# Performance work log

Measured on AMD Instinct MI355X. Metric: run time of the kernel, lower is better.

## Reference

```python
import jax, jax.numpy as jnp
import numpy as np

NU, NI = 16384, 8192          # num_users, num_items
DK, DM = 64, 64               # embed_k, embed_k_multimod
DV, DT = 4096, 384            # visual / textual feature dims
TOP_K = 10
N_LAYERS = 1                  # item-graph propagation layers
N_UI_LAYERS = 2               # user-item LGConv layers
L_M = 0.7
E = 524288                    # user-item interactions (doubled to symmetric edges)


def build_sim(x):
    # cosine similarity: row-normalize then x @ x.T  -> [N, N]
    xn = x / jnp.linalg.norm(x, axis=-1, keepdims=True)
    return xn @ xn.T


def build_knn(sim, k):
    # keep top-k values per row, zero elsewhere (torch topk + scatter_)
    vals, idx = jax.lax.top_k(sim, k)
    rows = jnp.arange(sim.shape[0])[:, None]
    return jnp.zeros_like(sim).at[rows, idx].set(vals)


def normalized_laplacian(adj):
    # D^{-1/2} A D^{-1/2}; inf (zero-degree) -> 0, applied as row/col scaling
    d = adj.sum(-1)
    dis = jnp.where(d > 0, jax.lax.rsqrt(jnp.where(d > 0, d, 1.0)), 0.0)
    return adj * dis[:, None] * dis[None, :]


def l2_normalize(x, axis=-1, eps=1e-12):
    n = jnp.linalg.norm(x, axis=axis, keepdims=True)
    return x / jnp.maximum(n, eps)


def setup_inputs() -> dict:
    key = jax.random.key(0)
    ks = jax.random.split(key, 8)
    Gu = jax.random.normal(ks[0], (NU, DK), jnp.float32) * 0.1
    Gi = jax.random.normal(ks[1], (NI, DK), jnp.float32) * 0.1
    feat_v = jax.random.normal(ks[2], (NI, DV), jnp.float32)
    feat_t = jax.random.normal(ks[3], (NI, DT), jnp.float32)
    W_v = jax.random.normal(ks[4], (DV, DM), jnp.float32) / np.sqrt(DV)
    b_v = jnp.zeros((DM,), jnp.float32)
    W_t = jax.random.normal(ks[5], (DT, DM), jnp.float32) / np.sqrt(DT)
    b_t = jnp.zeros((DM,), jnp.float32)
    importance_weights = jnp.full((2,), 0.5, jnp.float32)
    # precomputed per-modality normalized laplacians from raw (detached) features
    Sim_v = normalized_laplacian(build_knn(build_sim(feat_v), TOP_K))
    Sim_t = normalized_laplacian(build_knn(build_sim(feat_t), TOP_K))
    # symmetric bipartite user-item edge list (items offset by NU)
    u = jax.random.randint(ks[6], (E,), 0, NU)
    i = jax.random.randint(ks[7], (E,), 0, NI) + NU
    edge_index = jnp.stack([jnp.concatenate([u, i]), jnp.concatenate([i, u])])
    return dict(Gu=Gu, Gi=Gi, feat_v=feat_v, feat_t=feat_t, W_v=W_v, b_v=b_v,
                W_t=W_t, b_t=b_t, importance_weights=importance_weights,
                Sim_v=Sim_v, Sim_t=Sim_t, edge_index=edge_index)


def propagate(Gu, Gi, feat_v, feat_t, W_v, b_v, W_t, b_t,
              importance_weights, Sim_v, Sim_t, edge_index):
    w = jax.nn.softmax(importance_weights)
    learned = jnp.zeros((NI, NI), jnp.float32)
    original = jnp.zeros((NI, NI), jnp.float32)
    for m, (feat, W, b, Sim) in enumerate(
            [(feat_v, W_v, b_v, Sim_v), (feat_t, W_t, b_t, Sim_t)]):
        proj = feat @ W + b                                  # [NI, DM]
        learned = learned + w[m] * build_knn(build_sim(proj), TOP_K)
        original = original + w[m] * Sim
    Si = (1.0 - L_M) * normalized_laplacian(learned) + L_M * original
    # item-graph propagation
    item_emb = Gi
    for _ in range(N_LAYERS):
        item_emb = Si @ item_emb                              # [NI, DK]
    # user-item LGConv (normalize=False => plain sum aggregation)
    src, dst = edge_index[0], edge_index[1]
    all_emb = [jnp.concatenate([Gu, Gi], 0)]                  # [NU+NI, DK]
    for _ in range(N_UI_LAYERS):
        agg = jax.ops.segment_sum(all_emb[-1][src], dst, num_segments=NU + NI)
        all_emb.append(l2_normalize(agg, axis=1))
    mean_emb = jnp.stack(all_emb, 1).mean(1)
    gu, gi = mean_emb[:NU], mean_emb[NU:]
    return gu, gi + l2_normalize(item_emb, axis=1)


def reference(Gu, Gi, feat_v, feat_t, W_v, b_v, W_t, b_t,
              importance_weights, Sim_v, Sim_t, edge_index):
    return propagate(Gu, Gi, feat_v, feat_t, W_v, b_v, W_t, b_t,
                     importance_weights, Sim_v, Sim_t, edge_index)
```

## Files before the change

kernel.cpp:

```cpp
#include <hip/hip_runtime.h>
#include <hip/hip_bf16.h>

#define NU 16384
#define NI 8192
#define TOPK 10
#define NTOT (NU + NI)
#define OCAP 64
#define NSEG 4
#define CSEG (NI / NSEG)
#define NGRP 512
#define MAXSEL 16

typedef short short8v __attribute__((ext_vector_type(8)));
typedef float float4v __attribute__((ext_vector_type(4)));

__device__ __forceinline__ float warp64_sum(float v) {
#pragma unroll
  for (int m = 32; m >= 1; m >>= 1) v += __shfl_xor(v, m);
  return v;
}

__device__ __forceinline__ unsigned int umap(float f) {
  unsigned int b = __float_as_uint(f);
  return b ^ ((b & 0x80000000u) ? 0xFFFFFFFFu : 0x80000000u);
}

__global__ __launch_bounds__(256) void fused_proj_hist_kernel(
    const float* __restrict__ feat, const float* __restrict__ W,
    float* __restrict__ partial, int D, int kchunk,
    const int* __restrict__ dst, int* __restrict__ deg, int nedge) {
  __shared__ float sA[64][64];
  __shared__ float sB[64][68];
  const int tid = threadIdx.x;
  if (blockIdx.x >= 1024) {
    int e = (blockIdx.x - 1024) * 256 + tid;
    if (e < nedge) atomicAdd(&deg[dst[e]], 1);
    return;
  }
  const int pb = blockIdx.x;
  const int r0 = (pb & 127) * 64;
  const int ks = pb >> 7;
  const int rg = tid >> 4, cg = tid & 15;
  const int rA = tid & 63, kgA = (tid >> 6) * 16;
  const int kB = tid & 63, cbB = (tid >> 6) * 16;
  const int kbeg = ks * kchunk, kend = kbeg + kchunk;
  float4 pa[4], pb4[4];
  {
    const float* fp = feat + (size_t)(r0 + rA) * D + kbeg + kgA;
    pa[0] = *(const float4*)(fp + 0);  pa[1] = *(const float4*)(fp + 4);
    pa[2] = *(const float4*)(fp + 8);  pa[3] = *(const float4*)(fp + 12);
    const float* wp = W + (size_t)(kbeg + kB) * 64 + cbB;
    pb4[0] = *(const float4*)(wp + 0);  pb4[1] = *(const float4*)(wp + 4);
    pb4[2] = *(const float4*)(wp + 8);  pb4[3] = *(const float4*)(wp + 12);
  }
  float acc[4][4] = {{0,0,0,0},{0,0,0,0},{0,0,0,0},{0,0,0,0}};
  for (int kc = kbeg; kc < kend; kc += 64) {
#pragma unroll
    for (int i = 0; i < 4; ++i) {
      sA[kgA + 4*i + 0][rA] = pa[i].x;
      sA[kgA + 4*i + 1][rA] = pa[i].y;
      sA[kgA + 4*i + 2][rA] = pa[i].z;
      sA[kgA + 4*i + 3][rA] = pa[i].w;
      *(float4*)&sB[kB][cbB + 4*i] = pb4[i];
    }
    __syncthreads();
    if (kc + 64 < kend) {
      const float* fp = feat + (size_t)(r0 + rA) * D + kc + 64 + kgA;
      pa[0] = *(const float4*)(fp + 0);  pa[1] = *(const float4*)(fp + 4);
      pa[2] = *(const float4*)(fp + 8);  pa[3] = *(const float4*)(fp + 12);
      const float* wp = W + (size_t)(kc + 64 + kB) * 64 + cbB;
      pb4[0] = *(const float4*)(wp + 0);  pb4[1] = *(const float4*)(wp + 4);
      pb4[2] = *(const float4*)(wp + 8);  pb4[3] = *(const float4*)(wp + 12);
    }
#pragma unroll 8
    for (int k = 0; k < 64; ++k) {
      float4 a = *(const float4*)&sA[k][rg * 4];
      float4 b = *(const float4*)&sB[k][cg * 4];
      acc[0][0] += a.x * b.x; acc[0][1] += a.x * b.y; acc[0][2] += a.x * b.z; acc[0][3] += a.x * b.w;
      acc[1][0] += a.y * b.x; acc[1][1] += a.y * b.y; acc[1][2] += a.y * b.z; acc[1][3] += a.y * b.w;
      acc[2][0] += a.z * b.x; acc[2][1] += a.z * b.y; acc[2][2] += a.z * b.z; acc[2][3] += a.z * b.w;
      acc[3][0] += a.w * b.x; acc[3][1] += a.w * b.y; acc[3][2] += a.w * b.z; acc[3][3] += a.w * b.w;
    }
    __syncthreads();
  }
#pragma unroll
  for (int rr = 0; rr < 4; ++rr) {
    float4 o = make_float4(acc[rr][0], acc[rr][1], acc[rr][2], acc[rr][3]);
    *(float4*)(partial + ((size_t)ks * NI + r0 + rg * 4 + rr) * 64 + cg * 4) = o;
  }
}

__global__ __launch_bounds__(256) void fused_projT_reduceV_scanA_kernel(
    const float* __restrict__ feat, const float* __restrict__ W,
    float* __restrict__ partialT,
    const float* __restrict__ partialV, const float* __restrict__ bv,
    float* __restrict__ xn, ushort* __restrict__ hi, ushort* __restrict__ lo,
    const int* __restrict__ deg, int* __restrict__ loc, int* __restrict__ bsum) {
  __shared__ float sA[64][64];
  __shared__ float sB[64][68];
  __shared__ int s[256];
  const int tid = threadIdx.x;
  const int bid = blockIdx.x;
  if (bid >= 768 && bid < 2816) {
    const int row = (bid - 768) * 4 + (tid >> 6);
    const int col = tid & 63;
    float acc = bv[col];
#pragma unroll
    for (int ks = 0; ks < 8; ++ks)
      acc += partialV[((size_t)ks * NI + row) * 64 + col];
    float ss = warp64_sum(acc * acc);
    float v = acc * (1.0f / sqrtf(ss));
    xn[(size_t)row * 64 + col] = v;
    __hip_bfloat16 hb = __float2bfloat16(v);
    float hf = __bfloat162float(hb);
    __hip_bfloat16 lb = __float2bfloat16(v - hf);
    hi[(size_t)row * 64 + col] = *(ushort*)&hb;
    lo[(size_t)row * 64 + col] = *(ushort*)&lb;
    return;
  }
  if (bid >= 2816) {
    int gid = (bid - 2816) * 256 + tid;
    int x = deg[gid];
    s[tid] = x;
    __syncthreads();
    for (int off = 1; off < 256; off <<= 1) {
      int t = (tid >= off) ? s[tid - off] : 0;
      __syncthreads();
      s[tid] += t;
      __syncthreads();
    }
    loc[gid] = s[tid] - x;
    if (tid == 255) bsum[bid - 2816] = s[255];
    return;
  }
  const int pb = bid;
  const int r0 = (pb & 127) * 64;
  const int ks = pb >> 7;
  const int rg = tid >> 4, cg = tid & 15;
  const int rA = tid & 63, kgA = (tid >> 6) * 16;
  const int kB = tid & 63, cbB = (tid >> 6) * 16;
  const int kbeg = ks * 64;
  const int D = 384;
  float4 pa[4], pb4[4];
  {
    const float* fp = feat + (size_t)(r0 + rA) * D + kbeg + kgA;
    pa[0] = *(const float4*)(fp + 0);  pa[1] = *(const float4*)(fp + 4);
    pa[2] = *(const float4*)(fp + 8);  pa[3] = *(const float4*)(fp + 12);
    const float* wp = W + (size_t)(kbeg + kB) * 64 + cbB;
    pb4[0] = *(const float4*)(wp + 0);  pb4[1] = *(const float4*)(wp + 4);
    pb4[2] = *(const float4*)(wp + 8);  pb4[3] = *(const float4*)(wp + 12);
  }
  float acc[4][4] = {{0,0,0,0},{0,0,0,0},{0,0,0,0},{0,0,0,0}};
#pragma unroll
  for (int i = 0; i < 4; ++i) {
    sA[kgA + 4*i + 0][rA] = pa[i].x;
    sA[kgA + 4*i + 1][rA] = pa[i].y;
    sA[kgA + 4*i + 2][rA] = pa[i].z;
    sA[kgA + 4*i + 3][rA] = pa[i].w;
    *(float4*)&sB[kB][cbB + 4*i] = pb4[i];
  }
  __syncthreads();
#pragma unroll 8
  for (int k = 0; k < 64; ++k) {
    float4 a = *(const float4*)&sA[k][rg * 4];
    float4 b = *(const float4*)&sB[k][cg * 4];
    acc[0][0] += a.x * b.x; acc[0][1] += a.x * b.y; acc[0][2] += a.x * b.z; acc[0][3] += a.x * b.w;
    acc[1][0] += a.y * b.x; acc[1][1] += a.y * b.y; acc[1][2] += a.y * b.z; acc[1][3] += a.y * b.w;
    acc[2][0] += a.z * b.x; acc[2][1] += a.z * b.y; acc[2][2] += a.z * b.z; acc[2][3] += a.z * b.w;
    acc[3][0] += a.w * b.x; acc[3][1] += a.w * b.y; acc[3][2] += a.w * b.z; acc[3][3] += a.w * b.w;
  }
#pragma unroll
  for (int rr = 0; rr < 4; ++rr) {
    float4 o = make_float4(acc[rr][0], acc[rr][1], acc[rr][2], acc[rr][3]);
    *(float4*)(partialT + ((size_t)ks * NI + r0 + rg * 4 + rr) * 64 + cg * 4) = o;
  }
}

__global__ __launch_bounds__(256) void fused_reduceT_scanC_kernel(
    const float* __restrict__ partialT, const float* __restrict__ bt,
    float* __restrict__ xn, ushort* __restrict__ hi, ushort* __restrict__ lo,
    const int* __restrict__ loc, const int* __restrict__ bsum,
    int* __restrict__ row_ptr, int* __restrict__ cursor, int n) {
  const int tid = threadIdx.x;
  const int bid = blockIdx.x;
  if (bid >= 2048) {
    int gid = (bid - 2048) * 256 + tid;
    if (gid > n) return;
    int blk = gid >> 8;
    int off = 0;
    for (int b2 = 0; b2 < blk; ++b2) off += bsum[b2];
    if (gid == n) { row_ptr[n] = off; return; }
    int v = off + loc[gid];
    row_ptr[gid] = v;
    cursor[gid] = v;
    return;
  }
  const int row = bid * 4 + (tid >> 6);
  const int col = tid & 63;
  float acc = bt[col];
#pragma unroll
  for (int ks = 0; ks < 6; ++ks)
    acc += partialT[((size_t)ks * NI + row) * 64 + col];
  float ss = warp64_sum(acc * acc);
  float v = acc * (1.0f / sqrtf(ss));
  xn[(size_t)row * 64 + col] = v;
  __hip_bfloat16 hb = __float2bfloat16(v);
  float hf = __bfloat162float(hb);
  __hip_bfloat16 lb = __float2bfloat16(v - hf);
  hi[(size_t)row * 64 + col] = *(ushort*)&hb;
  lo[(size_t)row * 64 + col] = *(ushort*)&lb;
}

__global__ __launch_bounds__(256) void fused_sim_kernel(
    const float* __restrict__ Sv, const float* __restrict__ St,
    const float* __restrict__ iw, int* __restrict__ ocols,
    float* __restrict__ ow, int* __restrict__ ocnt,
    const ushort* __restrict__ hiV, const ushort* __restrict__ loV,
    const ushort* __restrict__ hiT, const ushort* __restrict__ loT,
    float* __restrict__ tmax,
    const int* __restrict__ esrc, const int* __restrict__ edst,
    int* __restrict__ cursor, int* __restrict__ csr, int nedge) {
  __shared__ ushort sH[64][64];
  __shared__ ushort sL[64][64];
  const int tid = threadIdx.x;
  const int bid = blockIdx.x;
  if (bid >= 1024 && bid < 3072) {
    const int lane = tid & 63;
    const int row = (bid - 1024) * 4 + (tid >> 6);
    float ea = expf(iw[0]), eb = expf(iw[1]);
    float wA = 0.7f * ea / (ea + eb), wB = 0.7f * eb / (ea + eb);
    int cnt = 0;
    int* oc = ocols + (size_t)row * OCAP;
    float* op = ow + (size_t)row * OCAP;
#pragma unroll 1
    for (int m = 0; m < 2; ++m) {
      const float* S = m ? St : Sv;
      float wgt = m ? wB : wA;
      const float4* rp = (const float4*)(S + (size_t)row * NI);
      float4 buf0 = rp[0 * 64 + lane];
      float4 buf1 = rp[1 * 64 + lane];
      float4 buf2 = rp[2 * 64 + lane];
      float4 buf3 = rp[3 * 64 + lane];
#pragma unroll 1
      for (int it0 = 0; it0 < NI / 256; it0 += 4) {
        float4 n0, n1, n2, n3;
        if (it0 + 4 < NI / 256) {
          n0 = rp[(it0 + 4) * 64 + lane];
          n1 = rp[(it0 + 5) * 64 + lane];
          n2 = rp[(it0 + 6) * 64 + lane];
          n3 = rp[(it0 + 7) * 64 + lane];
        }
#pragma unroll
        for (int k = 0; k < 4; ++k) {
          float4 cur = (k == 0) ? buf0 : (k == 1) ? buf1 : (k == 2) ? buf2 : buf3;
          const int it = it0 + k;
          bool anynz = (cur.x != 0.0f) | (cur.y != 0.0f) | (cur.z != 0.0f) | (cur.w != 0.0f);
          if (__ballot(anynz) != 0ull) {
            int cb = it * 256 + lane * 4;
#pragma unroll
            for (int j = 0; j < 4; ++j) {
              float x = (j == 0) ? cur.x : (j == 1) ? cur.y : (j == 2) ? cur.z : cur.w;
              bool nz = (x != 0.0f);
              unsigned long long mk = __ballot(nz);
              int pre = __popcll(mk & ((1ull << lane) - 1ull));
              if (nz) {
                int p = cnt + pre;
                if (p < OCAP) { oc[p] = cb + j; op[p] = wgt * x; }
              }
              cnt += __popcll(mk);
            }
          }
        }
        buf0 = n0; buf1 = n1; buf2 = n2; buf3 = n3;
      }
    }
    if (lane == 0) ocnt[row] = (cnt < OCAP) ? cnt : OCAP;
    return;
  }
  if (bid >= 3072) {
    int e = (bid - 3072) * 256 + tid;
    if (e < nedge) {
      int p = atomicAdd(&cursor[edst[e]], 1);
      csr[p] = esrc[e];
    }
    return;
  }
  const int t2 = bid;
  const int m = t2 >> 9;
  const int rest = t2 & 511;
  const int seg = rest >> 7;
  const int r_base = (rest & 127) * 64;
  const ushort* hi = m ? hiT : hiV;
  const ushort* lo = m ? loT : loV;
  const int c_base = seg * CSEG;
  const int wave = tid >> 6, lane = tid & 63;
  const int lr = lane & 15, lg = lane >> 4;
  const int my_row = r_base + wave * 16 + lr;
  short8v bh[2], bl[2];
  {
    const ushort* rp = hi + (size_t)my_row * 64 + lg * 8;
    bh[0] = *(const short8v*)(rp);
    bh[1] = *(const short8v*)(rp + 32);
    const ushort* rp2 = lo + (size_t)my_row * 64 + lg * 8;
    bl[0] = *(const short8v*)(rp2);
    bl[1] = *(const short8v*)(rp2 + 32);
  }
  float* tbase = tmax + ((size_t)m * NI + my_row) * NGRP + seg * (CSEG / 16);
  const int sc = tid >> 2, sq = (tid & 3) * 32;
  const int sw = (sc & 7) << 4;
  for (int c0 = 0; c0 < CSEG; c0 += 64) {
    __syncthreads();
    const char* gh = (const char*)(hi + (size_t)(c_base + c0 + sc) * 64);
    const char* gl2 = (const char*)(lo + (size_t)(c_base + c0 + sc) * 64);
    *(float4*)((char*)&sH[sc][0] + (sq ^ sw)) = *(const float4*)(gh + sq);
    *(float4*)((char*)&sH[sc][0] + ((sq + 16) ^ sw)) = *(const float4*)(gh + sq + 16);
    *(float4*)((char*)&sL[sc][0] + (sq ^ sw)) = *(const float4*)(gl2 + sq);
    *(float4*)((char*)&sL[sc][0] + ((sq + 16) ^ sw)) = *(const float4*)(gl2 + sq + 16);
    __syncthreads();
#pragma unroll
    for (int s = 0; s < 4; ++s) {
      const int ca = s * 16 + lr;
      const int cw = (ca & 7) << 4;
      const int kb0 = (lg * 16) ^ cw;
      const int kb1 = (lg * 16 + 64) ^ cw;
      short8v ah0 = *(const short8v*)((const char*)&sH[ca][0] + kb0);
      short8v ah1 = *(const short8v*)((const char*)&sH[ca][0] + kb1);
      short8v al0 = *(const short8v*)((const char*)&sL[ca][0] + kb0);
      short8v al1 = *(const short8v*)((const char*)&sL[ca][0] + kb1);
      float4v acc = {0.f, 0.f, 0.f, 0.f};
      acc = __builtin_amdgcn_mfma_f32_16x16x32_bf16(ah0, bh[0], acc, 0, 0, 0);
      acc = __builtin_amdgcn_mfma_f32_16x16x32_bf16(ah1, bh[1], acc, 0, 0, 0);
      acc = __builtin_amdgcn_mfma_f32_16x16x32_bf16(ah0, bl[0], acc, 0, 0, 0);
      acc = __builtin_amdgcn_mfma_f32_16x16x32_bf16(ah1, bl[1], acc, 0, 0, 0);
      acc = __builtin_amdgcn_mfma_f32_16x16x32_bf16(al0, bh[0], acc, 0, 0, 0);
      acc = __builtin_amdgcn_mfma_f32_16x16x32_bf16(al1, bh[1], acc, 0, 0, 0);
      float gm = fmaxf(fmaxf(acc[0], acc[1]), fmaxf(acc[2], acc[3]));
      gm = fmaxf(gm, __shfl_xor(gm, 16));
      gm = fmaxf(gm, __shfl_xor(gm, 32));
      if (lg == 0) tbase[(c0 >> 4) + s] = gm;
    }
  }
}

__global__ __launch_bounds__(256) void tile_rescore_kernel(
    const float* __restrict__ xn_v, const float* __restrict__ xn_t,
    const float* __restrict__ tmax,
    float* __restrict__ tkvV, int* __restrict__ tkiV,
    float* __restrict__ tkvT, int* __restrict__ tkiT) {
  const int bid = blockIdx.x;
  const int m = bid >> 13;
  const int row = bid & (NI - 1);
  const float* xn = m ? xn_t : xn_v;
  const int tid = threadIdx.x;
  __shared__ int ssel[MAXSEL];
  __shared__ float sval[MAXSEL * 16];
  __shared__ int scol[MAXSEL * 16];
  __shared__ float lv[32];
  __shared__ int lc[32];
  __shared__ int lnum;
  const int grp = tid >> 4, l16 = tid & 15;
  float4 rq = ((const float4*)(xn + (size_t)row * 64))[l16];
  if (tid < 64) {
    const int lane = tid;
    const float4* tmr4 = (const float4*)(tmax + ((size_t)m * NI + row) * NGRP);
    float4 t0 = tmr4[lane];
    float4 t1 = tmr4[64 + lane];
    unsigned int uv[8] = {umap(t0.x), umap(t0.y), umap(t0.z), umap(t0.w),
                          umap(t1.x), umap(t1.y), umap(t1.z), umap(t1.w)};
    unsigned long long blo = 0, bhi = 0x100000000ull;
    unsigned int taub = 0;
    for (int it = 0; it < 34; ++it) {
      unsigned int mid = (unsigned int)((blo + bhi) >> 1);
      int cnt = 0;
#pragma unroll
      for (int j = 0; j < 8; ++j) cnt += __popcll(__ballot(uv[j] >= mid));
      if (cnt >= 12) {
        taub = mid;
        if (cnt <= MAXSEL) break;
        blo = (unsigned long long)mid + 1;
      } else {
        bhi = mid;
      }
      if (blo >= bhi) break;
    }
    unsigned long long bj[8];
    int base[8];
    int tot = 0;
#pragma unroll
    for (int j = 0; j < 8; ++j) {
      bj[j] = __ballot(uv[j] >= taub);
      base[j] = tot;
      tot += __popcll(bj[j]);
    }
    if (lane < MAXSEL) ssel[lane] = -1;
    unsigned long long ltm = (1ull << lane) - 1ull;
#pragma unroll
    for (int j = 0; j < 8; ++j) {
      if (uv[j] >= taub) {
        int pos = base[j] + __popcll(bj[j] & ltm);
        if (pos < MAXSEL) {
          int g = (j < 4) ? (lane * 4 + j) : (256 + lane * 4 + (j - 4));
          ssel[pos] = g;
        }
      }
    }
  }
  __syncthreads();
  for (int it = 0; it < MAXSEL; ++it) {
    int gsel = ssel[it];
    bool valid = (gsel >= 0);
    int c = valid ? (gsel * 16 + grp) : 0;
    float4 x4 = ((const float4*)(xn + (size_t)c * 64))[l16];
    float s = rq.x * x4.x + rq.y * x4.y + rq.z * x4.z + rq.w * x4.w;
    s += __shfl_xor(s, 1);
    s += __shfl_xor(s, 2);
    s += __shfl_xor(s, 4);
    s += __shfl_xor(s, 8);
    if (l16 == 0) {
      sval[it * 16 + grp] = valid ? s : -3.0e38f;
      scol[it * 16 + grp] = valid ? c : 0x7fffffff;
    }
  }
  __syncthreads();
  if (tid < 64) {
    const int lane = tid;
    float fv[4];
    int fc[4];
    unsigned int uv4[4];
#pragma unroll
    for (int k = 0; k < 4; ++k) {
      fv[k] = sval[lane + 64 * k];
      fc[k] = scol[lane + 64 * k];
      uv4[k] = umap(fv[k]);
    }
    unsigned long long blo = 0, bhi = 0x100000000ull;
    unsigned int taub = 0;
    for (int it = 0; it < 34; ++it) {
      unsigned int mid = (unsigned int)((blo + bhi) >> 1);
      int cnt = 0;
#pragma unroll
      for (int k = 0; k < 4; ++k) cnt += __popcll(__ballot(uv4[k] >= mid));
      if (cnt >= TOPK) {
        taub = mid;
        if (cnt == TOPK) break;
        blo = (unsigned long long)mid + 1;
      } else {
        bhi = mid;
      }
      if (blo >= bhi) break;
    }
    unsigned long long bk[4];
    int base[4];
    int tot = 0;
#pragma unroll
    for (int k = 0; k < 4; ++k) {
      bk[k] = __ballot(uv4[k] >= taub);
      base[k] = tot;
      tot += __popcll(bk[k]);
    }
    float* tv = m ? tkvT : tkvV;
    int* ti = m ? tkiT : tkiV;
    unsigned long long ltm = (1ull << lane) - 1ull;
    if (tot == TOPK) {
#pragma unroll
      for (int k = 0; k < 4; ++k) {
        if (uv4[k] >= taub) {
          int pos = base[k] + __popcll(bk[k] & ltm);
          tv[(size_t)row * TOPK + pos] = fv[k];
          ti[(size_t)row * TOPK + pos] = fc[k];
        }
      }
    } else {
#pragma unroll
      for (int k = 0; k < 4; ++k) {
        if (uv4[k] >= taub) {
          int pos = base[k] + __popcll(bk[k] & ltm);
          if (pos < 32) { lv[pos] = fv[k]; lc[pos] = fc[k]; }
        }
      }
      if (lane == 0) lnum = (tot < 32) ? tot : 32;
      if (lane == 0) {
        int n = lnum;
        unsigned int used = 0;
        for (int q = 0; q < TOPK; ++q) {
          float bv = -3.0e38f;
          int bc = 0x7fffffff, bi = -1;
          for (int i2 = 0; i2 < n; ++i2) {
            if (used & (1u << i2)) continue;
            if (lv[i2] > bv || (lv[i2] == bv && lc[i2] < bc)) {
              bv = lv[i2]; bc = lc[i2]; bi = i2;
            }
          }
          used |= (1u << bi);
          tv[(size_t)row * TOPK + q] = bv;
          ti[(size_t)row * TOPK + q] = bc;
        }
      }
    }
  }
}

__global__ void dis_kernel(const float* __restrict__ tkv_v, const float* __restrict__ tkv_t,
                           const float* __restrict__ iw, float* __restrict__ dis) {
  int r = blockIdx.x * blockDim.x + threadIdx.x;
  if (r >= NI) return;
  float ea = expf(iw[0]), eb = expf(iw[1]);
  float w0 = ea / (ea + eb), w1 = eb / (ea + eb);
  float s0 = 0.f, s1 = 0.f;
  for (int j = 0; j < TOPK; ++j) { s0 += tkv_v[r * TOPK + j]; s1 += tkv_t[r * TOPK + j]; }
  float d = w0 * s0 + w1 * s1;
  dis[r] = (d > 0.0f) ? (1.0f / sqrtf(d)) : 0.0f;
}

__global__ __launch_bounds__(256) void fused_item_segsum_kernel(
    const float* __restrict__ Gi,
    const float* __restrict__ tkv_v, const int* __restrict__ tki_v,
    const float* __restrict__ tkv_t, const int* __restrict__ tki_t,
    const float* __restrict__ dis, const int* __restrict__ ocols,
    const float* __restrict__ ow, const int* __restrict__ ocnt,
    const float* __restrict__ iw, float* __restrict__ nitem,
    const float* __restrict__ Gu, const int* __restrict__ row_ptr,
    const int* __restrict__ csr, float* __restrict__ e1b) {
  const int tid = threadIdx.x;
  const int d = tid & 63;
  if (blockIdx.x >= 2048) {
    const int row = (blockIdx.x - 2048) * 4 + (tid >> 6);
    int a = row_ptr[row], bnd = row_ptr[row + 1];
    float acc = 0.0f;
    for (int e = a; e < bnd; ++e) {
      int s = csr[e];
      const float* sp = (s < NU) ? (Gu + (size_t)s * 64) : (Gi + (size_t)(s - NU) * 64);
      acc += sp[d];
    }
    float ss = warp64_sum(acc * acc);
    float nr = sqrtf(ss);
    e1b[(size_t)row * 64 + d] = acc / fmaxf(nr, 1e-12f);
    return;
  }
  const int row = blockIdx.x * 4 + (tid >> 6);
  float ea = expf(iw[0]), eb = expf(iw[1]);
  float w0 = ea / (ea + eb), w1 = eb / (ea + eb);
  float disr = dis[row];
  float acc = 0.0f;
#pragma unroll 1
  for (int m = 0; m < 2; ++m) {
    const float* tv = m ? tkv_t : tkv_v;
    const int* ti = m ? tki_t : tki_v;
    float wm = (m ? w1 : w0) * 0.3f * disr;
    for (int j = 0; j < TOPK; ++j) {
      float val = tv[(size_t)row * TOPK + j];
      int c = ti[(size_t)row * TOPK + j];
      acc += wm * val * dis[c] * Gi[(size_t)c * 64 + d];
    }
  }
  int cn = ocnt[row];
  for (int j = 0; j < cn; ++j) {
    int c = ocols[(size_t)row * OCAP + j];
    float wv = ow[(size_t)row * OCAP + j];
    acc += wv * Gi[(size_t)c * 64 + d];
  }
  float ss = warp64_sum(acc * acc);
  float nr = sqrtf(ss);
  nitem[(size_t)row * 64 + d] = acc / fmaxf(nr, 1e-12f);
}

__global__ __launch_bounds__(256) void segsum_final_kernel(
    const float* __restrict__ e1b, const int* __restrict__ row_ptr,
    const int* __restrict__ csr, const float* __restrict__ Gu,
    const float* __restrict__ Gi, const float* __restrict__ nitem,
    float* __restrict__ outp) {
  const int d = threadIdx.x & 63;
  const int row = blockIdx.x * 4 + (threadIdx.x >> 6);
  const float* inU = e1b;
  const float* inI = e1b + (size_t)NU * 64;
  int a = row_ptr[row], bnd = row_ptr[row + 1];
  float acc = 0.0f;
  for (int e = a; e < bnd; ++e) {
    int s = csr[e];
    const float* sp = (s < NU) ? (inU + (size_t)s * 64) : (inI + (size_t)(s - NU) * 64);
    acc += sp[d];
  }
  float ss = warp64_sum(acc * acc);
  float e2 = acc / fmaxf(sqrtf(ss), 1e-12f);
  float base = (row < NU) ? Gu[(size_t)row * 64 + d] : Gi[(size_t)(row - NU) * 64 + d];
  float v = (base + e1b[(size_t)row * 64 + d] + e2) * (1.0f / 3.0f);
  if (row >= NU) v += nitem[(size_t)(row - NU) * 64 + d];
  outp[(size_t)row * 64 + d] = v;
}

extern "C" void kernel_launch(void* const* d_in, const int* in_sizes, int n_in,
                              void* d_out, int out_size, void* d_ws, size_t ws_size,
                              hipStream_t stream) {
  const float* Gu = (const float*)d_in[0];
  const float* Gi = (const float*)d_in[1];
  const float* feat_v = (const float*)d_in[2];
  const float* feat_t = (const float*)d_in[3];
  const float* W_v = (const float*)d_in[4];
  const float* b_v = (const float*)d_in[5];
  const float* W_t = (const float*)d_in[6];
  const float* b_t = (const float*)d_in[7];
  const float* iw = (const float*)d_in[8];
  const float* Sv = (const float*)d_in[9];
  const float* St = (const float*)d_in[10];
  const int* eidx = (const int*)d_in[11];
  const int twoE = in_sizes[11] / 2;
  const int* esrc = eidx;
  const int* edst = eidx + twoE;
  float* outp = (float*)d_out;

  char* w = (char*)d_ws;
  size_t off = 0;
  auto alloc = [&](size_t bytes) -> void* {
    void* p = w + off;
    off = (off + bytes + 255) & ~(size_t)255;
    return p;
  };
  float* xn_v = (float*)alloc((size_t)NI * 64 * 4);
  float* xn_t = (float*)alloc((size_t)NI * 64 * 4);
  ushort* hiV = (ushort*)alloc((size_t)NI * 64 * 2);
  ushort* loV = (ushort*)alloc((size_t)NI * 64 * 2);
  ushort* hiT = (ushort*)alloc((size_t)NI * 64 * 2);
  ushort* loT = (ushort*)alloc((size_t)NI * 64 * 2);
  float* tmax = (float*)alloc((size_t)2 * NI * NGRP * 4);
  float* tkvV = (float*)alloc((size_t)NI * TOPK * 4);
  int* tkiV = (int*)alloc((size_t)NI * TOPK * 4);
  float* tkvT = (float*)alloc((size_t)NI * TOPK * 4);
  int* tkiT = (int*)alloc((size_t)NI * TOPK * 4);
  float* dis = (float*)alloc((size_t)NI * 4);
  int* ocols = (int*)alloc((size_t)NI * OCAP * 4);
  float* ow = (float*)alloc((size_t)NI * OCAP * 4);
  int* ocnt = (int*)alloc((size_t)NI * 4);
  float* nitem = (float*)alloc((size_t)NI * 64 * 4);
  float* e1b = (float*)alloc((size_t)NTOT * 64 * 4);
  int* deg = (int*)alloc((size_t)NTOT * 4);
  int* row_ptr = (int*)alloc((size_t)(NTOT + 1) * 4);
  int* cursor = (int*)alloc((size_t)NTOT * 4);
  int* csr = (int*)alloc((size_t)twoE * 4);
  int* locb = (int*)alloc((size_t)NTOT * 4);
  int* bsum = (int*)alloc((size_t)(NTOT / 256) * 4);
  if (off > ws_size) return;

  float* partialV = tmax;
  float* partialT = tmax + (size_t)8 * NI * 64;

  hipMemsetAsync(deg, 0, (size_t)NTOT * 4, stream);

  fused_proj_hist_kernel<<<1024 + 4096, 256, 0, stream>>>(
      feat_v, W_v, partialV, 4096, 512, edst, deg, twoE);
  fused_projT_reduceV_scanA_kernel<<<768 + 2048 + 96, 256, 0, stream>>>(
      feat_t, W_t, partialT, partialV, b_v, xn_v, hiV, loV, deg, locb, bsum);
  fused_reduceT_scanC_kernel<<<2048 + 97, 256, 0, stream>>>(
      partialT, b_t, xn_t, hiT, loT, locb, bsum, row_ptr, cursor, NTOT);
  fused_sim_kernel<<<1024 + 2048 + 4096, 256, 0, stream>>>(
      Sv, St, iw, ocols, ow, ocnt, hiV, loV, hiT, loT, tmax,
      esrc, edst, cursor, csr, twoE);
  tile_rescore_kernel<<<2 * NI, 256, 0, stream>>>(xn_v, xn_t, tmax, tkvV, tkiV,
                                                  tkvT, tkiT);
  dis_kernel<<<(NI + 255) / 256, 256, 0, stream>>>(tkvV, tkvT, iw, dis);
  fused_item_segsum_kernel<<<2048 + NTOT / 4, 256, 0, stream>>>(
      Gi, tkvV, tkiV, tkvT, tkiT, dis, ocols, ow, ocnt, iw, nitem,
      Gu, row_ptr, csr, e1b);
  segsum_final_kernel<<<NTOT / 4, 256, 0, stream>>>(e1b, row_ptr, csr, Gu, Gi, nitem, outp);
}
```

Before: 629.3 us.

## Split sim tile-max into its own kernel and fuse Sim scan with rescore

Moves the MFMA tile-max similarity computation into a dedicated kernel with 8 column segments instead of 4, giving 2048 blocks rather than 1024. The memory-bound scan of the precomputed Laplacians and the CSR fill move into the rescore kernel, interleaved one scan block per eight rescore blocks. The aim is to overlap bandwidth-heavy scanning with compute-heavy rescoring and to raise parallelism in the tile-max stage. The cost is extra per-block index arithmetic, and the finer segments shorten each block's loop, so the per-row B-fragment loads are amortized over less work.

```diff
diff --git a/kernel.cpp b/kernel.cpp
--- a/kernel.cpp
+++ b/kernel.cpp
@@ -6,8 +6,8 @@
 #define TOPK 10
 #define NTOT (NU + NI)
 #define OCAP 64
-#define NSEG 4
-#define CSEG (NI / NSEG)
+#define NSEG2 8
+#define CSEG2 (NI / NSEG2)
 #define NGRP 512
 #define MAXSEL 16
 
@@ -211,22 +211,94 @@
   lo[(size_t)row * 64 + col] = *(ushort*)&lb;
 }
 
-__global__ __launch_bounds__(256) void fused_sim_kernel(
-    const float* __restrict__ Sv, const float* __restrict__ St,
-    const float* __restrict__ iw, int* __restrict__ ocols,
-    float* __restrict__ ow, int* __restrict__ ocnt,
+__global__ __launch_bounds__(256) void sim_tilemax_kernel(
     const ushort* __restrict__ hiV, const ushort* __restrict__ loV,
     const ushort* __restrict__ hiT, const ushort* __restrict__ loT,
-    float* __restrict__ tmax,
-    const int* __restrict__ esrc, const int* __restrict__ edst,
-    int* __restrict__ cursor, int* __restrict__ csr, int nedge) {
+    float* __restrict__ tmax) {
   __shared__ ushort sH[64][64];
   __shared__ ushort sL[64][64];
   const int tid = threadIdx.x;
   const int bid = blockIdx.x;
-  if (bid >= 1024 && bid < 3072) {
+  const int m = bid >> 10;
+  const int rest = bid & 1023;
+  const int seg = rest >> 7;
+  const int r_base = (rest & 127) * 64;
+  const ushort* hi = m ? hiT : hiV;
+  const ushort* lo = m ? loT : loV;
+  const int c_base = seg * CSEG2;
+  const int wave = tid >> 6, lane = tid & 63;
+  const int lr = lane & 15, lg = lane >> 4;
+  const int my_row = r_base + wave * 16 + lr;
+  short8v bh[2], bl[2];
+  {
+    const ushort* rp = hi + (size_t)my_row * 64 + lg * 8;
+    bh[0] = *(const short8v*)(rp);
+    bh[1] = *(const short8v*)(rp + 32);
+    const ushort* rp2 = lo + (size_t)my_row * 64 + lg * 8;
+    bl[0] = *(const short8v*)(rp2);
+    bl[1] = *(const short8v*)(rp2 + 32);
+  }
+  float* tbase = tmax + ((size_t)m * NI + my_row) * NGRP + seg * (CSEG2 / 16);
+  const int sc = tid >> 2, sq = (tid & 3) * 32;
+  const int sw = (sc & 7) << 4;
+  for (int c0 = 0; c0 < CSEG2; c0 += 64) {
+    __syncthreads();
+    const char* gh = (const char*)(hi + (size_t)(c_base + c0 + sc) * 64);
+    const char* gl2 = (const char*)(lo + (size_t)(c_base + c0 + sc) * 64);
+    *(float4*)((char*)&sH[sc][0] + (sq ^ sw)) = *(const float4*)(gh + sq);
+    *(float4*)((char*)&sH[sc][0] + ((sq + 16) ^ sw)) = *(const float4*)(gh + sq + 16);
+    *(float4*)((char*)&sL[sc][0] + (sq ^ sw)) = *(const float4*)(gl2 + sq);
+    *(float4*)((char*)&sL[sc][0] + ((sq + 16) ^ sw)) = *(const float4*)(gl2 + sq + 16);
+    __syncthreads();
+#pragma unroll
+    for (int s = 0; s < 4; ++s) {
+      const int ca = s * 16 + lr;
+      const int cw = (ca & 7) << 4;
+      const int kb0 = (lg * 16) ^ cw;
+      const int kb1 = (lg * 16 + 64) ^ cw;
+      short8v ah0 = *(const short8v*)((const char*)&sH[ca][0] + kb0);
+      short8v ah1 = *(const short8v*)((const char*)&sH[ca][0] + kb1);
+      short8v al0 = *(const short8v*)((const char*)&sL[ca][0] + kb0);
+      short8v al1 = *(const short8v*)((const char*)&sL[ca][0] + kb1);
+      float4v acc = {0.f, 0.f, 0.f, 0.f};
+      acc = __builtin_amdgcn_mfma_f32_16x16x32_bf16(ah0, bh[0], acc, 0, 0, 0);
+      acc = __builtin_amdgcn_mfma_f32_16x16x32_bf16(ah1, bh[1], acc, 0, 0, 0);
+      acc = __builtin_amdgcn_mfma_f32_16x16x32_bf16(ah0, bl[0], acc, 0, 0, 0);
+      acc = __builtin_amdgcn_mfma_f32_16x16x32_bf16(ah1, bl[1], acc, 0, 0, 0);
+      acc = __builtin_amdgcn_mfma_f32_16x16x32_bf16(al0, bh[0], acc, 0, 0, 0);
+      acc = __builtin_amdgcn_mfma_f32_16x16x32_bf16(al1, bh[1], acc, 0, 0, 0);
+      float gm = fmaxf(fmaxf(acc[0], acc[1]), fmaxf(acc[2], acc[3]));
+      gm = fmaxf(gm, __shfl_xor(gm, 16));
+      gm = fmaxf(gm, __shfl_xor(gm, 32));
+      if (lg == 0) tbase[(c0 >> 4) + s] = gm;
+    }
+  }
+}
+
+__global__ __launch_bounds__(256) void fused_scan_rescore_fill_kernel(
+    const float* __restrict__ Sv, const float* __restrict__ St,
+    const float* __restrict__ iw, int* __restrict__ ocols,
+    float* __restrict__ ow, int* __restrict__ ocnt,
+    const float* __restrict__ xn_v, const float* __restrict__ xn_t,
+    const float* __restrict__ tmax,
+    float* __restrict__ tkvV, int* __restrict__ tkiV,
+    float* __restrict__ tkvT, int* __restrict__ tkiT,
+    const int* __restrict__ esrc, const int* __restrict__ edst,
+    int* __restrict__ cursor, int* __restrict__ csr, int nedge) {
+  const int tid = threadIdx.x;
+  const int bid0 = blockIdx.x;
+  if (bid0 >= 18432) {
+    int e = (bid0 - 18432) * 256 + tid;
+    if (e < nedge) {
+      int p = atomicAdd(&cursor[edst[e]], 1);
+      csr[p] = esrc[e];
+    }
+    return;
+  }
+  const int sgrp = bid0 / 9;
+  if (bid0 % 9 == 0) {
     const int lane = tid & 63;
-    const int row = (bid - 1024) * 4 + (tid >> 6);
+    const int row = sgrp * 4 + (tid >> 6);
     float ea = expf(iw[0]), eb = expf(iw[1]);
     float wA = 0.7f * ea / (ea + eb), wB = 0.7f * eb / (ea + eb);
     int cnt = 0;
@@ -277,81 +349,10 @@
     if (lane == 0) ocnt[row] = (cnt < OCAP) ? cnt : OCAP;
     return;
   }
-  if (bid >= 3072) {
-    int e = (bid - 3072) * 256 + tid;
-    if (e < nedge) {
-      int p = atomicAdd(&cursor[edst[e]], 1);
-      csr[p] = esrc[e];
-    }
-    return;
-  }
-  const int t2 = bid;
-  const int m = t2 >> 9;
-  const int rest = t2 & 511;
-  const int seg = rest >> 7;
-  const int r_base = (rest & 127) * 64;
-  const ushort* hi = m ? hiT : hiV;
-  const ushort* lo = m ? loT : loV;
-  const int c_base = seg * CSEG;
-  const int wave = tid >> 6, lane = tid & 63;
-  const int lr = lane & 15, lg = lane >> 4;
-  const int my_row = r_base + wave * 16 + lr;
-  short8v bh[2], bl[2];
-  {
-    const ushort* rp = hi + (size_t)my_row * 64 + lg * 8;
-    bh[0] = *(const short8v*)(rp);
-    bh[1] = *(const short8v*)(rp + 32);
-    const ushort* rp2 = lo + (size_t)my_row * 64 + lg * 8;
-    bl[0] = *(const short8v*)(rp2);
-    bl[1] = *(const short8v*)(rp2 + 32);
-  }
-  float* tbase = tmax + ((size_t)m * NI + my_row) * NGRP + seg * (CSEG / 16);
-  const int sc = tid >> 2, sq = (tid & 3) * 32;
-  const int sw = (sc & 7) << 4;
-  for (int c0 = 0; c0 < CSEG; c0 += 64) {
-    __syncthreads();
-    const char* gh = (const char*)(hi + (size_t)(c_base + c0 + sc) * 64);
-    const char* gl2 = (const char*)(lo + (size_t)(c_base + c0 + sc) * 64);
-    *(float4*)((char*)&sH[sc][0] + (sq ^ sw)) = *(const float4*)(gh + sq);
-    *(float4*)((char*)&sH[sc][0] + ((sq + 16) ^ sw)) = *(const float4*)(gh + sq + 16);
-    *(float4*)((char*)&sL[sc][0] + (sq ^ sw)) = *(const float4*)(gl2 + sq);
-    *(float4*)((char*)&sL[sc][0] + ((sq + 16) ^ sw)) = *(const float4*)(gl2 + sq + 16);
-    __syncthreads();
-#pragma unroll
-    for (int s = 0; s < 4; ++s) {
-      const int ca = s * 16 + lr;
-      const int cw = (ca & 7) << 4;
-      const int kb0 = (lg * 16) ^ cw;
-      const int kb1 = (lg * 16 + 64) ^ cw;
-      short8v ah0 = *(const short8v*)((const char*)&sH[ca][0] + kb0);
-      short8v ah1 = *(const short8v*)((const char*)&sH[ca][0] + kb1);
-      short8v al0 = *(const short8v*)((const char*)&sL[ca][0] + kb0);
-      short8v al1 = *(const short8v*)((const char*)&sL[ca][0] + kb1);
-      float4v acc = {0.f, 0.f, 0.f, 0.f};
-      acc = __builtin_amdgcn_mfma_f32_16x16x32_bf16(ah0, bh[0], acc, 0, 0, 0);
-      acc = __builtin_amdgcn_mfma_f32_16x16x32_bf16(ah1, bh[1], acc, 0, 0, 0);
-      acc = __builtin_amdgcn_mfma_f32_16x16x32_bf16(ah0, bl[0], acc, 0, 0, 0);
-      acc = __builtin_amdgcn_mfma_f32_16x16x32_bf16(ah1, bl[1], acc, 0, 0, 0);
-      acc = __builtin_amdgcn_mfma_f32_16x16x32_bf16(al0, bh[0], acc, 0, 0, 0);
-      acc = __builtin_amdgcn_mfma_f32_16x16x32_bf16(al1, bh[1], acc, 0, 0, 0);
-      float gm = fmaxf(fmaxf(acc[0], acc[1]), fmaxf(acc[2], acc[3]));
-      gm = fmaxf(gm, __shfl_xor(gm, 16));
-      gm = fmaxf(gm, __shfl_xor(gm, 32));
-      if (lg == 0) tbase[(c0 >> 4) + s] = gm;
-    }
-  }
-}
-
-__global__ __launch_bounds__(256) void tile_rescore_kernel(
-    const float* __restrict__ xn_v, const float* __restrict__ xn_t,
-    const float* __restrict__ tmax,
-    float* __restrict__ tkvV, int* __restrict__ tkiV,
-    float* __restrict__ tkvT, int* __restrict__ tkiT) {
-  const int bid = blockIdx.x;
+  const int bid = bid0 - sgrp - 1;
   const int m = bid >> 13;
   const int row = bid & (NI - 1);
   const float* xn = m ? xn_t : xn_v;
-  const int tid = threadIdx.x;
   __shared__ int ssel[MAXSEL];
   __shared__ float sval[MAXSEL * 16];
   __shared__ int scol[MAXSEL * 16];
@@ -651,11 +652,10 @@
       feat_t, W_t, partialT, partialV, b_v, xn_v, hiV, loV, deg, locb, bsum);
   fused_reduceT_scanC_kernel<<<2048 + 97, 256, 0, stream>>>(
       partialT, b_t, xn_t, hiT, loT, locb, bsum, row_ptr, cursor, NTOT);
-  fused_sim_kernel<<<1024 + 2048 + 4096, 256, 0, stream>>>(
-      Sv, St, iw, ocols, ow, ocnt, hiV, loV, hiT, loT, tmax,
+  sim_tilemax_kernel<<<2048, 256, 0, stream>>>(hiV, loV, hiT, loT, tmax);
+  fused_scan_rescore_fill_kernel<<<18432 + 4096, 256, 0, stream>>>(
+      Sv, St, iw, ocols, ow, ocnt, xn_v, xn_t, tmax, tkvV, tkiV, tkvT, tkiT,
       esrc, edst, cursor, csr, twoE);
-  tile_rescore_kernel<<<2 * NI, 256, 0, stream>>>(xn_v, xn_t, tmax, tkvV, tkiV,
-                                                  tkvT, tkiT);
   dis_kernel<<<(NI + 255) / 256, 256, 0, stream>>>(tkvV, tkvT, iw, dis);
   fused_item_segsum_kernel<<<2048 + NTOT / 4, 256, 0, stream>>>(
       Gi, tkvV, tkiV, tkvT, tkiT, dis, ocols, ow, ocnt, iw, nitem,
```

After: 608.1 us (median of 3 runs). 3.4% less time.
